# Kernel tuning notes

Hardware: AMD Instinct MI355X
Metric: run time of the kernel (lower is better)

The kernel has to match this reference:

```python
import jax, jax.numpy as jnp
import numpy as np

# Config
V = 32000        # Y_vocab_size
EMB = 512        # decoder_embedding_size
ENC_H = 1024     # encoder_hidden_size
DEC_H = 1024     # decoder_hidden_size
ATT = 512        # attention_size
L = 2            # num_decoder_layers
B, T, S = 32, 64, 128


def setup_inputs() -> dict:
    key = jax.random.key(0)
    ks = jax.random.split(key, 20)
    s = 0.02
    emb = jax.random.normal(ks[3], (V, EMB), jnp.float32) * s
    emb = emb.at[0].set(0.0)  # padding_idx=0 row is zeros
    return {
        "y_decoder_input": jax.random.randint(ks[0], (B, T), 0, V),
        "encoder_outputs": jax.random.normal(ks[1], (B, S, ENC_H), jnp.float32),
        "decoder_init_hidden": jax.random.normal(ks[2], (L, B, DEC_H), jnp.float32),
        "encoder_mask": jnp.ones((B, S), jnp.int32),
        "emb_table": emb,
        "W_enc": jax.random.normal(ks[4], (ATT, ENC_H), jnp.float32) * s,
        "W_dec": jax.random.normal(ks[5], (ATT, DEC_H), jnp.float32) * s,
        "v_w": jax.random.normal(ks[6], (ATT,), jnp.float32) * s,
        "W_ih0": jax.random.normal(ks[7], (DEC_H, EMB + ENC_H), jnp.float32) * s,
        "W_hh0": jax.random.normal(ks[8], (DEC_H, DEC_H), jnp.float32) * s,
        "b_ih0": jax.random.normal(ks[9], (DEC_H,), jnp.float32) * s,
        "b_hh0": jax.random.normal(ks[10], (DEC_H,), jnp.float32) * s,
        "W_ih1": jax.random.normal(ks[11], (DEC_H, DEC_H), jnp.float32) * s,
        "W_hh1": jax.random.normal(ks[12], (DEC_H, DEC_H), jnp.float32) * s,
        "b_ih1": jax.random.normal(ks[13], (DEC_H,), jnp.float32) * s,
        "b_hh1": jax.random.normal(ks[14], (DEC_H,), jnp.float32) * s,
        "fc_w": jax.random.normal(ks[15], (V - 1, DEC_H), jnp.float32) * s,
        "fc_b": jnp.zeros((V - 1,), jnp.float32),
    }


def reference(y_decoder_input, encoder_outputs, decoder_init_hidden, encoder_mask,
              emb_table, W_enc, W_dec, v_w,
              W_ih0, W_hh0, b_ih0, b_hh0, W_ih1, W_hh1, b_ih1, b_hh1,
              fc_w, fc_b):
    embedded = emb_table[y_decoder_input]                       # [B,T,EMB]
    enc_proj = jnp.einsum('bse,ae->bsa', encoder_outputs, W_enc)  # hoisted (same math each step)
    pad_mask = (encoder_mask == 0)                              # [B,S]

    def step(hidden, emb_t):
        prev = hidden[-1]                                       # [B,DEC_H] top layer
        dec_p = prev @ W_dec.T                                  # [B,ATT]
        scores = jnp.tanh(enc_proj + dec_p[:, None, :]) @ v_w   # [B,S]
        scores = jnp.where(pad_mask, jnp.float32(-1e9), scores)
        attn = jax.nn.softmax(scores, axis=-1)                  # [B,S]
        context = jnp.einsum('bs,bse->be', attn, encoder_outputs)  # [B,ENC_H]
        x = jnp.concatenate([emb_t, context], axis=1)           # [B,EMB+ENC_H]
        h0 = jnp.tanh(x @ W_ih0.T + b_ih0 + hidden[0] @ W_hh0.T + b_hh0)
        h1 = jnp.tanh(h0 @ W_ih1.T + b_ih1 + hidden[1] @ W_hh1.T + b_hh1)
        out = h1 @ fc_w.T + fc_b                                # [B,V-1]
        return jnp.stack([h0, h1]), (out, attn)

    _, (outs, attns) = jax.lax.scan(step, decoder_init_hidden,
                                    jnp.swapaxes(embedded, 0, 1))  # scan over T
    outputs = jnp.swapaxes(outs, 0, 1)                          # [B,T,V-1]
    attn_weights = jnp.swapaxes(attns, 0, 1)                    # [B,T,S]
    return outputs, attn_weights
```

## Files before the change

kernel.cpp:

```cpp
#include <hip/hip_runtime.h>

typedef unsigned short u16;
typedef unsigned int u32;
typedef __attribute__((ext_vector_type(8))) short bf16x8;
typedef __attribute__((ext_vector_type(4))) float f32x4;
typedef __attribute__((ext_vector_type(2))) unsigned int u32x2;

#define MFMA_BF16(a,b,c) __builtin_amdgcn_mfma_f32_16x16x32_bf16((a),(b),(c),0,0,0)

__device__ __forceinline__ u16 f2bf(float f) {
  union { float f; u32 u; } v; v.f = f;
  u32 r = v.u + 0x7FFFu + ((v.u >> 16) & 1u);
  return (u16)(r >> 16);
}
__device__ __forceinline__ float bf2f(u16 h) {
  union { u32 u; float f; } v; v.u = ((u32)h) << 16; return v.f;
}
__device__ __forceinline__ float tanh_fast(float x) {
  float e = __expf(2.0f * x);
  return 1.0f - 2.0f / (e + 1.0f);
}
__device__ __forceinline__ float exp2_fast(float x) {
  float r; asm("v_exp_f32 %0, %1" : "=v"(r) : "v"(x)); return r;
}
__device__ __forceinline__ float rcp_fast(float x) {
  float r; asm("v_rcp_f32 %0, %1" : "=v"(r) : "v"(x)); return r;
}

__device__ __forceinline__ void issue_lcoh(bf16x8& v, const u16* p) {
  asm volatile("global_load_dwordx4 %0, %1, off sc0 sc1" : "=v"(v) : "v"(p));
}
__device__ __forceinline__ void vm_wait0() {
  asm volatile("s_waitcnt vmcnt(0)" ::: "memory");
  __builtin_amdgcn_sched_barrier(0);
}
__device__ __forceinline__ void scoh_u32(u32* p, u32 v) {
  asm volatile("global_store_dword %0, %1, off sc0 sc1" :: "v"(p), "v"(v) : "memory");
}
__device__ __forceinline__ void scoh_dx2(u16* p, u32 lo, u32 hi) {
  u32x2 v; v.x = lo; v.y = hi;
  asm volatile("global_store_dwordx2 %0, %1, off sc0 sc1" :: "v"(p), "v"(v) : "memory");
}
__device__ __forceinline__ void scoh_dx4(u16* p, bf16x8 v) {
  asm volatile("global_store_dwordx4 %0, %1, off sc0 sc1" :: "v"(p), "v"(v) : "memory");
}
__device__ __forceinline__ u32 poll_load(const u32* p) {
  u32 v;
  asm volatile("global_load_dword %0, %1, off sc0 sc1\n\ts_waitcnt vmcnt(0)"
               : "=v"(v) : "v"(p) : "memory");
  return v;
}

__device__ __forceinline__ void poll_flags(const u32* base, int P, u32 target) {
  if (target == 0u) return;
  if ((threadIdx.x >> 6) == 0) {
    const int lane = threadIdx.x & 63;
    const u32* s0 = base + (size_t)(lane & (P - 1)) * 32;
    for (;;) {
      u32 v0 = poll_load(s0);
      if (__all(v0 >= target)) break;
      __builtin_amdgcn_s_sleep(1);
    }
  }
  __syncthreads();
  __builtin_amdgcn_sched_barrier(0);
}
__device__ __forceinline__ void post_flag(u32* slot, u32 val) {
  asm volatile("s_waitcnt vmcnt(0)" ::: "memory");
  __syncthreads();
  if (threadIdx.x == 0) scoh_u32(slot, val);
}

__global__ void prep_kernel(
    const float* __restrict__ fcw, const float* __restrict__ enc,
    const float* __restrict__ wenc, const float* __restrict__ wdec,
    const float* __restrict__ wih0, const float* __restrict__ whh0,
    const float* __restrict__ wih1, const float* __restrict__ whh1,
    const float* __restrict__ bih0, const float* __restrict__ bhh0,
    const float* __restrict__ bih1, const float* __restrict__ bhh1,
    const float* __restrict__ emb, const int* __restrict__ yin,
    const float* __restrict__ dih,
    u16* __restrict__ fcwb, u16* __restrict__ encb, u16* __restrict__ wencb,
    u16* __restrict__ wdecb, u16* __restrict__ w0eh, u16* __restrict__ w0ctx,
    u16* __restrict__ w1cat, u16* __restrict__ embbt,
    float* __restrict__ bias0, float* __restrict__ bias1,
    u16* __restrict__ h0buf0, u16* __restrict__ h1buf0)
{
  const float SCL = 2.8853900817779268f;
  const long long total = 43845632LL;
  for (long long i = (long long)blockIdx.x * 256 + threadIdx.x; i < total;
       i += (long long)gridDim.x * 256) {
    if (i < 32768000LL) {
      int r = (int)(i >> 10), c = (int)(i & 1023);
      fcwb[i] = (r < 31999) ? f2bf(fcw[(long long)r * 1024 + c]) : (u16)0;
    } else if (i < 36962304LL) {
      long long j = i - 32768000LL; encb[j] = f2bf(enc[j]);
    } else if (i < 37486592LL) {
      long long j = i - 36962304LL; wencb[j] = f2bf(wenc[j] * SCL);
    } else if (i < 38010880LL) {
      long long j = i - 37486592LL; wdecb[j] = f2bf(wdec[j] * SCL);
    } else if (i < 39583744LL) {
      long long j = i - 38010880LL;
      int r = (int)(j / 1536), c = (int)(j % 1536);
      float v = (c < 512) ? wih0[(long long)r * 1536 + c]
                          : whh0[(long long)r * 1024 + (c - 512)];
      w0eh[j] = f2bf(v);
    } else if (i < 40632320LL) {
      long long j = i - 39583744LL;
      int r = (int)(j >> 10), e = (int)(j & 1023);
      w0ctx[j] = f2bf(wih0[(long long)r * 1536 + 512 + e]);
    } else if (i < 42729472LL) {
      long long j = i - 40632320LL;
      int r = (int)(j >> 11), c = (int)(j & 2047);
      w1cat[j] = f2bf(c < 1024 ? wih1[(r << 10) + c] : whh1[(r << 10) + (c - 1024)]);
    } else if (i < 43778048LL) {
      long long j = i - 42729472LL;
      int bt = (int)(j >> 9), c = (int)(j & 511);
      int y = yin[bt];
      embbt[j] = f2bf(emb[(long long)y * 512 + c]);
    } else if (i < 43779072LL) {
      int j = (int)(i - 43778048LL); bias0[j] = bih0[j] + bhh0[j];
    } else if (i < 43780096LL) {
      int j = (int)(i - 43779072LL); bias1[j] = bih1[j] + bhh1[j];
    } else if (i < 43812864LL) {
      int j = (int)(i - 43780096LL); h0buf0[j] = f2bf(dih[j]);
    } else {
      int j = (int)(i - 43812864LL); h1buf0[j] = f2bf(dih[32768 + j]);
    }
  }
}

template <int OUT16>
__global__ __launch_bounds__(256) void gemm128(
    const u16* __restrict__ A, const u16* __restrict__ Bm,
    const float* __restrict__ bias, void* __restrict__ Cv,
    int K, int ldc, int Nvalid, int ntN)
{
  __shared__ u16 As[128 * 32];
  __shared__ u16 Bs[128 * 32];
  const int tid = threadIdx.x;
  const int bid = blockIdx.x;
  const int tM = bid / ntN, tN = bid - tM * ntN;
  const int m0 = tM * 128, n0 = tN * 128;
  const int lane = tid & 63, wid = tid >> 6;
  const int wm = wid >> 1, wn = wid & 1;
  const int srow = tid >> 1, scol = (tid & 1) * 16;

  const u16* gA = A + (size_t)(m0 + srow) * K + scol;
  const u16* gB = Bm + (size_t)(n0 + srow) * K + scol;
  u16* sA = &As[srow * 32 + scol];
  u16* sB = &Bs[srow * 32 + scol];

  f32x4 acc[4][4];
#pragma unroll
  for (int i = 0; i < 4; ++i)
#pragma unroll
    for (int j = 0; j < 4; ++j) acc[i][j] = (f32x4){0, 0, 0, 0};

  const int aoff = (wm * 64 + (lane & 15)) * 32 + ((lane >> 4) << 3);
  const int boff = (wn * 64 + (lane & 15)) * 32 + ((lane >> 4) << 3);

  for (int k0 = 0; k0 < K; k0 += 32) {
    bf16x8 va0 = *(const bf16x8*)(gA + k0);
    bf16x8 va1 = *(const bf16x8*)(gA + k0 + 8);
    bf16x8 vb0 = *(const bf16x8*)(gB + k0);
    bf16x8 vb1 = *(const bf16x8*)(gB + k0 + 8);
    __syncthreads();
    *((bf16x8*)sA) = va0;  *((bf16x8*)(sA + 8)) = va1;
    *((bf16x8*)sB) = vb0;  *((bf16x8*)(sB + 8)) = vb1;
    __syncthreads();
    bf16x8 af[4], bfj[4];
#pragma unroll
    for (int i = 0; i < 4; ++i) af[i] = *(const bf16x8*)&As[aoff + i * 512];
#pragma unroll
    for (int j = 0; j < 4; ++j) bfj[j] = *(const bf16x8*)&Bs[boff + j * 512];
#pragma unroll
    for (int i = 0; i < 4; ++i)
#pragma unroll
      for (int j = 0; j < 4; ++j)
        acc[i][j] = MFMA_BF16(af[i], bfj[j], acc[i][j]);
  }

#pragma unroll
  for (int i = 0; i < 4; ++i) {
#pragma unroll
    for (int j = 0; j < 4; ++j) {
      int row = m0 + wm * 64 + i * 16 + ((lane >> 4) << 2);
      int cc = n0 + wn * 64 + j * 16 + (lane & 15);
      if (cc < Nvalid) {
        float bs = bias ? bias[cc] : 0.f;
#pragma unroll
        for (int jj = 0; jj < 4; ++jj) {
          if (OUT16)
            ((u16*)Cv)[(size_t)(row + jj) * ldc + cc] = f2bf(acc[i][j][jj] + bs);
          else
            ((float*)Cv)[(size_t)(row + jj) * ldc + cc] = acc[i][j][jj] + bs;
        }
      }
    }
  }
}

__global__ __launch_bounds__(512, 1) void decoder_persistent(
    const u16* __restrict__ wdecb, const u16* __restrict__ w0eh,
    const u16* __restrict__ w1cat, const u16* __restrict__ encprojb,
    const u16* __restrict__ encW0T, const u16* __restrict__ embbt,
    const float* __restrict__ bias0, const float* __restrict__ bias1,
    const float* __restrict__ vw, const int* __restrict__ msk,
    u16* __restrict__ partials, u16* __restrict__ attbufB,
    u16* __restrict__ h0buf, u16* __restrict__ h1buf,
    u16* __restrict__ h1all, float* __restrict__ outattn, u32* flags)
{
  extern __shared__ char smem[];
  const int tid = threadIdx.x;
  const int bid = blockIdx.x;
  const int lane = tid & 63, wid = tid >> 6;
  const int l15 = lane & 15, l16 = (lane >> 4) << 3;
  const f32x4 zero4 = {0, 0, 0, 0};
  u32* h1flags = flags;
  u32* scflags = flags + 32 * 32;
  u32* h0flags = flags + 64 * 32;

  if (bid < 32) {
    const int n0 = bid * 32;
    u16* w1L = (u16*)smem;
    float* scr = (float*)(smem + 131584);
    u16* h1newL = (u16*)(smem + 147968);
    float* b1L = (float*)(smem + 150016);
    {
      for (int c = tid; c < 8192; c += 512) {
        int r = c >> 8, seg = (c & 255) * 8;
        *(bf16x8*)&w1L[r * 2056 + seg] =
            *(const bf16x8*)&w1cat[(size_t)(n0 + r) * 2048 + seg];
      }
      if (tid < 32) b1L[tid] = bias1[n0 + tid];
      for (int c = tid; c < 1024; c += 512) {
        int b = c >> 5, n = c & 31;
        h1newL[c] = h1buf[(size_t)b * 1024 + n0 + n];
      }
    }
    __syncthreads();
    const int bt = wid >> 2, kq = wid & 3;
    const int ab = bt * 16 + l15;

    for (int t = -1; t < 64; ++t) {
      if (t >= 0) {
        poll_flags(h1flags, 32, (u32)(t + 1));
        const u16* hp = h1buf + (size_t)(t & 1) * 32768;
        f32x4 acc0 = zero4, acc1 = zero4;
        {
          bf16x8 av[8];
#pragma unroll
          for (int ks = 0; ks < 8; ++ks)
            issue_lcoh(av[ks], hp + (size_t)ab * 1024 + kq * 256 + ks * 32 + l16);
          vm_wait0();
#pragma unroll
          for (int ks = 0; ks < 8; ++ks) {
            int kx = 1024 + kq * 256 + ks * 32 + l16;
            acc0 = MFMA_BF16(av[ks], *(const bf16x8*)&w1L[l15 * 2056 + kx], acc0);
            acc1 = MFMA_BF16(av[ks], *(const bf16x8*)&w1L[(16 + l15) * 2056 + kx], acc1);
          }
        }
        poll_flags(h0flags, 64, (u32)(t + 1));
        const u16* hn = h0buf + (size_t)((t + 1) & 1) * 32768;
        {
          bf16x8 av[8];
#pragma unroll
          for (int ks = 0; ks < 8; ++ks)
            issue_lcoh(av[ks], hn + (size_t)ab * 1024 + kq * 256 + ks * 32 + l16);
          vm_wait0();
#pragma unroll
          for (int ks = 0; ks < 8; ++ks) {
            int kx = kq * 256 + ks * 32 + l16;
            acc0 = MFMA_BF16(av[ks], *(const bf16x8*)&w1L[l15 * 2056 + kx], acc0);
            acc1 = MFMA_BF16(av[ks], *(const bf16x8*)&w1L[(16 + l15) * 2056 + kx], acc1);
          }
        }
        *(f32x4*)&scr[((wid * 2 + 0) * 64 + lane) * 4] = acc0;
        *(f32x4*)&scr[((wid * 2 + 1) * 64 + lane) * 4] = acc1;
        __syncthreads();
        {
          int b = tid >> 4, n16 = tid & 15;
          int lanep = (((b & 15) >> 2) << 4) | n16;
          int r = b & 3, btc = b >> 4;
#pragma unroll
          for (int nt = 0; nt < 2; ++nt) {
            int n = nt * 16 + n16;
            float s = b1L[n];
#pragma unroll
            for (int q = 0; q < 4; ++q)
              s += scr[(((btc * 4 + q) * 2 + nt) * 64 + lanep) * 4 + r];
            h1newL[b * 32 + n] = f2bf(tanh_fast(s));
          }
        }
        __syncthreads();
        if (tid < 128) {
          int b = tid >> 2, q = tid & 3;
          bf16x8 v8 = *(const bf16x8*)&h1newL[b * 32 + q * 8];
          scoh_dx4(h1buf + (size_t)((t + 1) & 1) * 32768 + (size_t)b * 1024 + n0 + q * 8, v8);
          *(bf16x8*)(h1all + ((size_t)b * 64 + t) * 1024 + n0 + q * 8) = v8;
        }
      }
      {
#pragma unroll
        for (int bt2 = 0; bt2 < 2; ++bt2) {
          bf16x8 hb = *(const bf16x8*)&h1newL[(bt2 * 16 + l15) * 32 + l16];
#pragma unroll
          for (int i = 0; i < 4; ++i) {
            int at = wid * 4 + i;
            bf16x8 wa = *(const bf16x8*)&wdecb[(size_t)(at * 16 + l15) * 1024 + n0 + l16];
            f32x4 c = MFMA_BF16(wa, hb, zero4);
            int a0 = at * 16 + ((lane >> 4) << 2);
            int bb = bt2 * 16 + l15;
            u32 lo = (u32)f2bf(c[0]) | ((u32)f2bf(c[1]) << 16);
            u32 hi = (u32)f2bf(c[2]) | ((u32)f2bf(c[3]) << 16);
            scoh_dx2(partials + ((size_t)bb * 32 + bid) * 512 + a0, lo, hi);
          }
        }
      }
      post_flag(h1flags + (size_t)bid * 32, (u32)(t + 2));
    }
  } else if (bid < 64) {
    const int b = bid - 32;
    u16* epL = (u16*)smem;
    float* vwL = (float*)(smem + 133120);
    float* red = (float*)(smem + 135168);
    float* decpL = (float*)(smem + 151552);
    float* attF = (float*)(smem + 153600);
    u16* attB = (u16*)(smem + 154112);
    float* eL = (float*)(smem + 154368);
    float* mkL = (float*)(smem + 154880);
    float* sumL = (float*)(smem + 155392);
    {
      for (int c = tid; c < 8192; c += 512)
        *(bf16x8*)&epL[(c >> 6) * 520 + (c & 63) * 8] =
            *(const bf16x8*)&encprojb[((size_t)b * 128 + (c >> 6)) * 512 + (c & 63) * 8];
      vwL[tid] = vw[tid];
      if (tid < 128) mkL[tid] = (float)msk[b * 128 + tid];
    }
    __syncthreads();
    for (int t = 0; t < 64; ++t) {
      poll_flags(h1flags, 32, (u32)(t + 1));
      {
        const int a8 = tid & 63, hg = tid >> 6;
        const int a = a8 * 8;
        bf16x8 w[4];
#pragma unroll
        for (int i = 0; i < 4; ++i)
          issue_lcoh(w[i], partials + ((size_t)b * 32 + hg * 4 + i) * 512 + a);
        vm_wait0();
        float s[8];
#pragma unroll
        for (int e = 0; e < 8; ++e) {
          s[e] = bf2f((u16)w[0][e]) + bf2f((u16)w[1][e]) +
                 bf2f((u16)w[2][e]) + bf2f((u16)w[3][e]);
        }
#pragma unroll
        for (int e = 0; e < 8; ++e) red[hg * 512 + a + e] = s[e];
      }
      __syncthreads();
      {
        float s = 0.f;
#pragma unroll
        for (int hg = 0; hg < 8; ++hg) s += red[hg * 512 + tid];
        decpL[tid] = s;
      }
      __syncthreads();
      {
        const int s = tid >> 2, q = tid & 3;
        const u16* ep = &epL[s * 520 + q * 128];
        const float* dp = &decpL[q * 128];
        const float* vv = &vwL[q * 128];
        float a0 = 0.f, a1 = 0.f;
#pragma unroll
        for (int ii = 0; ii < 16; ++ii) {
          int i = (ii + q * 4) & 15;
          bf16x8 ev = *(const bf16x8*)(ep + i * 8);
#pragma unroll
          for (int e = 0; e < 8; e += 2) {
            float x0 = bf2f((u16)ev[e]) + dp[i * 8 + e];
            float x1 = bf2f((u16)ev[e + 1]) + dp[i * 8 + e + 1];
            a0 = fmaf(vv[i * 8 + e],     1.f - 2.f * rcp_fast(exp2_fast(x0) + 1.f), a0);
            a1 = fmaf(vv[i * 8 + e + 1], 1.f - 2.f * rcp_fast(exp2_fast(x1) + 1.f), a1);
          }
        }
        float acc = a0 + a1;
        acc += __shfl_xor(acc, 1);
        acc += __shfl_xor(acc, 2);
        float e = 0.f;
        if (q == 0) { e = (mkL[s] != 0.f) ? __expf(acc) : 0.f; eL[s] = e; }
        float ee = e;
#pragma unroll
        for (int off = 1; off < 64; off <<= 1) ee += __shfl_xor(ee, off);
        if (lane == 0) sumL[wid] = ee;
      }
      __syncthreads();
      {
        float tot = sumL[0] + sumL[1] + sumL[2] + sumL[3] +
                    sumL[4] + sumL[5] + sumL[6] + sumL[7];
        if (tid < 128) {
          float att = (tot > 0.f) ? eL[tid] * rcp_fast(tot) : 0.0078125f;
          attF[tid] = att;
          attB[tid] = f2bf(att);
        }
      }
      __syncthreads();
      if (tid < 32)
        *(f32x4*)(outattn + ((size_t)b * 64 + t) * 128 + tid * 4) = *(const f32x4*)&attF[tid * 4];
      if (tid < 16)
        scoh_dx4(attbufB + (size_t)b * 128 + tid * 8, *(const bf16x8*)&attB[tid * 8]);
      post_flag(scflags + (size_t)b * 32, (u32)(t + 1));
    }
  } else {
    const int h = bid - 64, j0 = h * 16;
    u16* e0L = (u16*)smem;
    float* attL = (float*)(smem + 131328);
    float* scrH = (float*)(smem + 147712);
    u16* h0newL = (u16*)(smem + 155904);
    float* b0L = (float*)(smem + 156928);
    {
      for (int c = tid; c < 8192; c += 512) {
        int j = c >> 9, off = (c & 511) * 8;
        *(bf16x8*)&e0L[j * 4104 + off] =
            *(const bf16x8*)&encW0T[(size_t)(j0 + j) * 4096 + off];
      }
      if (tid < 16) b0L[tid] = bias0[j0 + tid];
    }
    __syncthreads();
    const int bt = wid >> 2, kq = wid & 3;
    const int ab = bt * 16 + l15;

    for (int t = 0; t < 64; ++t) {
      poll_flags(h0flags, 64, (u32)t);
      {
        bf16x8 xa[12], wb[12];
        const u16* hp = h0buf + (size_t)(t & 1) * 32768;
#pragma unroll
        for (int ks = 0; ks < 12; ++ks) {
          int kk = kq * 384 + ks * 32;
          if (kk < 512)
            xa[ks] = *(const bf16x8*)&embbt[((size_t)ab * 64 + t) * 512 + kk + l16];
          else
            issue_lcoh(xa[ks], hp + (size_t)ab * 1024 + (kk - 512) + l16);
          wb[ks] = *(const bf16x8*)&w0eh[(size_t)(j0 + l15) * 1536 + kk + l16];
        }
        vm_wait0();
        f32x4 acc = zero4;
#pragma unroll
        for (int ks = 0; ks < 12; ++ks) acc = MFMA_BF16(xa[ks], wb[ks], acc);
        *(f32x4*)&scrH[(wid * 64 + lane) * 4] = acc;
      }
      poll_flags(scflags, 32, (u32)(t + 1));
      {
        bf16x8 v;
        issue_lcoh(v, attbufB + tid * 8);
        vm_wait0();
#pragma unroll
        for (int e = 0; e < 8; ++e) attL[tid * 8 + e] = bf2f((u16)v[e]);
      }
      __syncthreads();
      {
        int b = tid >> 4, j = tid & 15;
        const float* ar = &attL[b * 128];
        float adot = 0.f;
#pragma unroll
        for (int c8 = 0; c8 < 16; ++c8) {
          bf16x8 ev = *(const bf16x8*)&e0L[j * 4104 + b * 128 + c8 * 8];
#pragma unroll
          for (int e = 0; e < 8; ++e) adot = fmaf(ar[c8 * 8 + e], bf2f((u16)ev[e]), adot);
        }
        int lanep = (((b & 15) >> 2) << 4) | j;
        int r = b & 3, btc = b >> 4;
        float s = adot + b0L[j];
#pragma unroll
        for (int q = 0; q < 4; ++q)
          s += scrH[((btc * 4 + q) * 64 + lanep) * 4 + r];
        h0newL[b * 16 + j] = f2bf(tanh_fast(s));
      }
      __syncthreads();
      if (tid < 64) {
        int b = tid >> 1, half = tid & 1;
        scoh_dx4(h0buf + (size_t)((t + 1) & 1) * 32768 + (size_t)b * 1024 + j0 + half * 8,
                 *(const bf16x8*)&h0newL[b * 16 + half * 8]);
      }
      post_flag(h0flags + (size_t)h * 32, (u32)(t + 1));
    }
  }
}

extern "C" void kernel_launch(void* const* d_in, const int* in_sizes, int n_in,
                              void* d_out, int out_size, void* d_ws, size_t ws_size,
                              hipStream_t stream)
{
  const int*   yin  = (const int*)d_in[0];
  const float* enc  = (const float*)d_in[1];
  const float* dih  = (const float*)d_in[2];
  const int*   msk  = (const int*)d_in[3];
  const float* emb  = (const float*)d_in[4];
  const float* wenc = (const float*)d_in[5];
  const float* wdec = (const float*)d_in[6];
  const float* vw   = (const float*)d_in[7];
  const float* wih0 = (const float*)d_in[8];
  const float* whh0 = (const float*)d_in[9];
  const float* bih0 = (const float*)d_in[10];
  const float* bhh0 = (const float*)d_in[11];
  const float* wih1 = (const float*)d_in[12];
  const float* whh1 = (const float*)d_in[13];
  const float* bih1 = (const float*)d_in[14];
  const float* bhh1 = (const float*)d_in[15];
  const float* fcw  = (const float*)d_in[16];
  const float* fcb  = (const float*)d_in[17];

  char* ws = (char*)d_ws;
  size_t off = 0;
  auto alloc = [&](size_t bytes) {
    char* p = ws + off; off += (bytes + 255) & ~(size_t)255; return p;
  };
  u16*   fcwb     = (u16*)alloc(32768000ULL * 2);
  u16*   encb     = (u16*)alloc(4194304ULL * 2);
  u16*   wencb    = (u16*)alloc(524288ULL * 2);
  u16*   wdecb    = (u16*)alloc(524288ULL * 2);
  u16*   w0eh     = (u16*)alloc(1572864ULL * 2);
  u16*   w0ctx    = (u16*)alloc(1048576ULL * 2);
  u16*   w1cat    = (u16*)alloc(2097152ULL * 2);
  u16*   embbt    = (u16*)alloc(1048576ULL * 2);
  u16*   encprojb = (u16*)alloc(2097152ULL * 2);
  u16*   encW0T   = (u16*)alloc(4194304ULL * 2);
  u16*   partials = (u16*)alloc(524288ULL * 2);
  u16*   attbufB  = (u16*)alloc(4096ULL * 2);
  u16*   h0buf    = (u16*)alloc(65536ULL * 2);
  u16*   h1buf    = (u16*)alloc(65536ULL * 2);
  u16*   h1all    = (u16*)alloc(2097152ULL * 2);
  float* bias0    = (float*)alloc(1024ULL * 4);
  float* bias1    = (float*)alloc(1024ULL * 4);
  u32*   flags    = (u32*)alloc(16384ULL);
  if (off > ws_size) return;

  float* outlog  = (float*)d_out;
  float* outattn = outlog + 65533952ULL;

  (void)hipMemsetAsync(flags, 0, 16384, stream);

  prep_kernel<<<2048, 256, 0, stream>>>(
      fcw, enc, wenc, wdec, wih0, whh0, wih1, whh1,
      bih0, bhh0, bih1, bhh1, emb, yin, dih,
      fcwb, encb, wencb, wdecb, w0eh, w0ctx, w1cat, embbt, bias0, bias1,
      h0buf, h1buf);

  gemm128<1><<<32 * 4, 256, 0, stream>>>(encb, wencb, nullptr, encprojb,
                                         1024, 512, 512, 4);
  gemm128<1><<<8 * 32, 256, 0, stream>>>(w0ctx, encb, nullptr, encW0T,
                                         1024, 4096, 4096, 32);

  (void)hipFuncSetAttribute((const void*)decoder_persistent,
                            hipFuncAttributeMaxDynamicSharedMemorySize, 157184);
  decoder_persistent<<<128, 512, 157184, stream>>>(
      wdecb, w0eh, w1cat, encprojb, encW0T, embbt, bias0, bias1,
      vw, msk, partials, attbufB, h0buf, h1buf, h1all, outattn, flags);

  gemm128<0><<<16 * 250, 256, 0, stream>>>(h1all, fcwb, fcb, outlog,
                                           1024, 31999, 31999, 250);
}
```

Before: 1.933 ms.

## Fuse output projection into persistent decoder as extra overlapping blocks

```diff
diff --git a/kernel.cpp b/kernel.cpp
--- a/kernel.cpp
+++ b/kernel.cpp
@@ -87,54 +87,52 @@
     u16* __restrict__ h0buf0, u16* __restrict__ h1buf0)
 {
   const float SCL = 2.8853900817779268f;
-  const long long total = 43845632LL;
+  const long long total = 44632064LL;
   for (long long i = (long long)blockIdx.x * 256 + threadIdx.x; i < total;
        i += (long long)gridDim.x * 256) {
-    if (i < 32768000LL) {
+    if (i < 33554432LL) {
       int r = (int)(i >> 10), c = (int)(i & 1023);
       fcwb[i] = (r < 31999) ? f2bf(fcw[(long long)r * 1024 + c]) : (u16)0;
-    } else if (i < 36962304LL) {
-      long long j = i - 32768000LL; encb[j] = f2bf(enc[j]);
-    } else if (i < 37486592LL) {
-      long long j = i - 36962304LL; wencb[j] = f2bf(wenc[j] * SCL);
-    } else if (i < 38010880LL) {
-      long long j = i - 37486592LL; wdecb[j] = f2bf(wdec[j] * SCL);
-    } else if (i < 39583744LL) {
-      long long j = i - 38010880LL;
+    } else if (i < 37748736LL) {
+      long long j = i - 33554432LL; encb[j] = f2bf(enc[j]);
+    } else if (i < 38273024LL) {
+      long long j = i - 37748736LL; wencb[j] = f2bf(wenc[j] * SCL);
+    } else if (i < 38797312LL) {
+      long long j = i - 38273024LL; wdecb[j] = f2bf(wdec[j] * SCL);
+    } else if (i < 40370176LL) {
+      long long j = i - 38797312LL;
       int r = (int)(j / 1536), c = (int)(j % 1536);
       float v = (c < 512) ? wih0[(long long)r * 1536 + c]
                           : whh0[(long long)r * 1024 + (c - 512)];
       w0eh[j] = f2bf(v);
-    } else if (i < 40632320LL) {
-      long long j = i - 39583744LL;
+    } else if (i < 41418752LL) {
+      long long j = i - 40370176LL;
       int r = (int)(j >> 10), e = (int)(j & 1023);
       w0ctx[j] = f2bf(wih0[(long long)r * 1536 + 512 + e]);
-    } else if (i < 42729472LL) {
-      long long j = i - 40632320LL;
+    } else if (i < 43515904LL) {
+      long long j = i - 41418752LL;
       int r = (int)(j >> 11), c = (int)(j & 2047);
       w1cat[j] = f2bf(c < 1024 ? wih1[(r << 10) + c] : whh1[(r << 10) + (c - 1024)]);
-    } else if (i < 43778048LL) {
-      long long j = i - 42729472LL;
+    } else if (i < 44564480LL) {
+      long long j = i - 43515904LL;
       int bt = (int)(j >> 9), c = (int)(j & 511);
       int y = yin[bt];
       embbt[j] = f2bf(emb[(long long)y * 512 + c]);
-    } else if (i < 43779072LL) {
-      int j = (int)(i - 43778048LL); bias0[j] = bih0[j] + bhh0[j];
-    } else if (i < 43780096LL) {
-      int j = (int)(i - 43779072LL); bias1[j] = bih1[j] + bhh1[j];
-    } else if (i < 43812864LL) {
-      int j = (int)(i - 43780096LL); h0buf0[j] = f2bf(dih[j]);
+    } else if (i < 44565504LL) {
+      int j = (int)(i - 44564480LL); bias0[j] = bih0[j] + bhh0[j];
+    } else if (i < 44566528LL) {
+      int j = (int)(i - 44565504LL); bias1[j] = bih1[j] + bhh1[j];
+    } else if (i < 44599296LL) {
+      int j = (int)(i - 44566528LL); h0buf0[j] = f2bf(dih[j]);
     } else {
-      int j = (int)(i - 43812864LL); h1buf0[j] = f2bf(dih[32768 + j]);
+      int j = (int)(i - 44599296LL); h1buf0[j] = f2bf(dih[32768 + j]);
     }
   }
 }
 
-template <int OUT16>
-__global__ __launch_bounds__(256) void gemm128(
+__global__ __launch_bounds__(256) void gemm128b(
     const u16* __restrict__ A, const u16* __restrict__ Bm,
-    const float* __restrict__ bias, void* __restrict__ Cv,
-    int K, int ldc, int Nvalid, int ntN)
+    u16* __restrict__ Cv, int K, int ldc, int ntN)
 {
   __shared__ u16 As[128 * 32];
   __shared__ u16 Bs[128 * 32];
@@ -187,16 +185,9 @@
     for (int j = 0; j < 4; ++j) {
       int row = m0 + wm * 64 + i * 16 + ((lane >> 4) << 2);
       int cc = n0 + wn * 64 + j * 16 + (lane & 15);
-      if (cc < Nvalid) {
-        float bs = bias ? bias[cc] : 0.f;
-#pragma unroll
-        for (int jj = 0; jj < 4; ++jj) {
-          if (OUT16)
-            ((u16*)Cv)[(size_t)(row + jj) * ldc + cc] = f2bf(acc[i][j][jj] + bs);
-          else
-            ((float*)Cv)[(size_t)(row + jj) * ldc + cc] = acc[i][j][jj] + bs;
-        }
-      }
+#pragma unroll
+      for (int jj = 0; jj < 4; ++jj)
+        Cv[(size_t)(row + jj) * ldc + cc] = f2bf(acc[i][j][jj]);
     }
   }
 }
@@ -207,9 +198,11 @@
     const u16* __restrict__ encW0T, const u16* __restrict__ embbt,
     const float* __restrict__ bias0, const float* __restrict__ bias1,
     const float* __restrict__ vw, const int* __restrict__ msk,
+    const u16* __restrict__ fcwb, const float* __restrict__ fcb,
     u16* __restrict__ partials, u16* __restrict__ attbufB,
     u16* __restrict__ h0buf, u16* __restrict__ h1buf,
-    u16* __restrict__ h1all, float* __restrict__ outattn, u32* flags)
+    u16* __restrict__ h1all, float* __restrict__ outattn,
+    float* __restrict__ outlog, u32* flags)
 {
   extern __shared__ char smem[];
   const int tid = threadIdx.x;
@@ -298,7 +291,7 @@
           int b = tid >> 2, q = tid & 3;
           bf16x8 v8 = *(const bf16x8*)&h1newL[b * 32 + q * 8];
           scoh_dx4(h1buf + (size_t)((t + 1) & 1) * 32768 + (size_t)b * 1024 + n0 + q * 8, v8);
-          *(bf16x8*)(h1all + ((size_t)b * 64 + t) * 1024 + n0 + q * 8) = v8;
+          scoh_dx4(h1all + ((size_t)b * 64 + t) * 1024 + n0 + q * 8, v8);
         }
       }
       {
@@ -349,14 +342,10 @@
         for (int i = 0; i < 4; ++i)
           issue_lcoh(w[i], partials + ((size_t)b * 32 + hg * 4 + i) * 512 + a);
         vm_wait0();
-        float s[8];
-#pragma unroll
-        for (int e = 0; e < 8; ++e) {
-          s[e] = bf2f((u16)w[0][e]) + bf2f((u16)w[1][e]) +
-                 bf2f((u16)w[2][e]) + bf2f((u16)w[3][e]);
-        }
-#pragma unroll
-        for (int e = 0; e < 8; ++e) red[hg * 512 + a + e] = s[e];
+#pragma unroll
+        for (int e = 0; e < 8; ++e)
+          red[hg * 512 + a + e] = bf2f((u16)w[0][e]) + bf2f((u16)w[1][e]) +
+                                  bf2f((u16)w[2][e]) + bf2f((u16)w[3][e]);
       }
       __syncthreads();
       {
@@ -411,7 +400,7 @@
         scoh_dx4(attbufB + (size_t)b * 128 + tid * 8, *(const bf16x8*)&attB[tid * 8]);
       post_flag(scflags + (size_t)b * 32, (u32)(t + 1));
     }
-  } else {
+  } else if (bid < 128) {
     const int h = bid - 64, j0 = h * 16;
     u16* e0L = (u16*)smem;
     float* attL = (float*)(smem + 131328);
@@ -484,6 +473,67 @@
                  *(const bf16x8*)&h0newL[b * 16 + half * 8]);
       }
       post_flag(h0flags + (size_t)h * 32, (u32)(t + 1));
+    }
+  } else {
+    const int f = bid - 128;
+    const int n0g = f * 256;
+    u16* aL = (u16*)smem;
+    for (int t = 0; t < 64; ++t) {
+      if ((tid >> 6) == 0) {
+        const u32* s0 = h1flags + (size_t)(lane & 31) * 32;
+        for (;;) {
+          u32 v0 = poll_load(s0);
+          if (__all(v0 >= (u32)(t + 2))) break;
+          __builtin_amdgcn_s_sleep(8);
+        }
+      }
+      __syncthreads();
+      __builtin_amdgcn_sched_barrier(0);
+      {
+        int b = tid >> 4, ks = (tid & 15) * 64;
+        bf16x8 v[8];
+        const u16* src = h1all + ((size_t)b * 64 + t) * 1024 + ks;
+#pragma unroll
+        for (int i = 0; i < 8; ++i) issue_lcoh(v[i], src + i * 8);
+        vm_wait0();
+#pragma unroll
+        for (int i = 0; i < 8; ++i) *(bf16x8*)&aL[b * 1024 + ks + i * 8] = v[i];
+      }
+      __syncthreads();
+      f32x4 acc00 = zero4, acc01 = zero4, acc10 = zero4, acc11 = zero4;
+      const int nt0 = wid * 2;
+      const u16* brow0 = fcwb + (size_t)(n0g + (nt0 + 0) * 16 + l15) * 1024;
+      const u16* brow1 = fcwb + (size_t)(n0g + (nt0 + 1) * 16 + l15) * 1024;
+#pragma unroll 4
+      for (int kk = 0; kk < 32; ++kk) {
+        int ko = kk * 32 + l16;
+        bf16x8 a0 = *(const bf16x8*)&aL[l15 * 1024 + ko];
+        bf16x8 a1 = *(const bf16x8*)&aL[(16 + l15) * 1024 + ko];
+        bf16x8 b0 = *(const bf16x8*)(brow0 + ko);
+        bf16x8 b1 = *(const bf16x8*)(brow1 + ko);
+        acc00 = MFMA_BF16(a0, b0, acc00);
+        acc10 = MFMA_BF16(a1, b0, acc10);
+        acc01 = MFMA_BF16(a0, b1, acc01);
+        acc11 = MFMA_BF16(a1, b1, acc11);
+      }
+      __syncthreads();
+      {
+        const int rq = (lane >> 4) << 2;
+#pragma unroll
+        for (int ntl = 0; ntl < 2; ++ntl) {
+          int col = n0g + (nt0 + ntl) * 16 + l15;
+          if (col < 31999) {
+            float bs = fcb[col];
+            f32x4 c0 = ntl ? acc01 : acc00;
+            f32x4 c1 = ntl ? acc11 : acc10;
+#pragma unroll
+            for (int j = 0; j < 4; ++j) {
+              outlog[(size_t)((rq + j) * 64 + t) * 31999 + col] = c0[j] + bs;
+              outlog[(size_t)((16 + rq + j) * 64 + t) * 31999 + col] = c1[j] + bs;
+            }
+          }
+        }
+      }
     }
   }
 }
@@ -516,7 +566,7 @@
   auto alloc = [&](size_t bytes) {
     char* p = ws + off; off += (bytes + 255) & ~(size_t)255; return p;
   };
-  u16*   fcwb     = (u16*)alloc(32768000ULL * 2);
+  u16*   fcwb     = (u16*)alloc(33554432ULL * 2);
   u16*   encb     = (u16*)alloc(4194304ULL * 2);
   u16*   wencb    = (u16*)alloc(524288ULL * 2);
   u16*   wdecb    = (u16*)alloc(524288ULL * 2);
@@ -547,17 +597,13 @@
       fcwb, encb, wencb, wdecb, w0eh, w0ctx, w1cat, embbt, bias0, bias1,
       h0buf, h1buf);
 
-  gemm128<1><<<32 * 4, 256, 0, stream>>>(encb, wencb, nullptr, encprojb,
-                                         1024, 512, 512, 4);
-  gemm128<1><<<8 * 32, 256, 0, stream>>>(w0ctx, encb, nullptr, encW0T,
-                                         1024, 4096, 4096, 32);
+  gemm128b<<<32 * 4, 256, 0, stream>>>(encb, wencb, encprojb, 1024, 512, 4);
+  gemm128b<<<8 * 32, 256, 0, stream>>>(w0ctx, encb, encW0T, 1024, 4096, 32);
 
   (void)hipFuncSetAttribute((const void*)decoder_persistent,
                             hipFuncAttributeMaxDynamicSharedMemorySize, 157184);
-  decoder_persistent<<<128, 512, 157184, stream>>>(
+  decoder_persistent<<<256, 512, 157184, stream>>>(
       wdecb, w0eh, w1cat, encprojb, encW0T, embbt, bias0, bias1,
-      vw, msk, partials, attbufB, h0buf, h1buf, h1all, outattn, flags);
-
-  gemm128<0><<<16 * 250, 256, 0, stream>>>(h1all, fcwb, fcb, outlog,
-                                           1024, 31999, 31999, 250);
-}
+      vw, msk, fcwb, fcb, partials, attbufB, h0buf, h1buf, h1all,
+      outattn, outlog, flags);
+}
```

After: 1.631 ms (median of 2 runs). 1.18x faster.
